# Kernel optimization log

Measured on AMD Instinct MI355X. Metric: run time of the kernel, lower is better.

The kernel has to match this reference:

```python
import jax, jax.numpy as jnp
import numpy as np

N = 200000      # total nodes
E = 3200000     # total edges (avg degree 16)
B = 2000        # graphs
NPG = 100       # nodes per graph (N = B*NPG)
H = 32          # hidden_channels
MAXZ = 1000     # max_z
K = 60          # sort-pool k
D = H * 3 + 1   # total_latent_dim = 97
DENSE = ((K - 2) // 2 + 1 - 5 + 1) * 32  # 832


def setup_inputs() -> dict:
    key = jax.random.key(0)
    ks = jax.random.split(key, 24)
    inp = {}
    inp['z1'] = jax.random.randint(ks[0], (N,), 0, MAXZ)
    inp['z2'] = jax.random.randint(ks[1], (N,), 0, MAXZ)
    inp['w'] = jax.random.randint(ks[2], (N,), 0, MAXZ)
    inp['edge_index'] = jax.random.randint(ks[3], (2, E), 0, N)
    inp['batch'] = jnp.arange(N) // NPG  # contiguous graph ids
    inp['edge_weight'] = jax.random.uniform(ks[4], (E,), dtype=jnp.float32)
    s = 0.1
    inp['emb_w'] = jax.random.normal(ks[5], (MAXZ, H), jnp.float32) * s
    inp['emb_z1'] = jax.random.normal(ks[6], (MAXZ, H), jnp.float32) * s
    inp['emb_z2'] = jax.random.normal(ks[7], (MAXZ, H), jnp.float32) * s
    inp['W0'] = jax.random.normal(ks[8], (3 * H, H), jnp.float32) * s
    inp['b0'] = jnp.zeros((H,), jnp.float32)
    inp['W1'] = jax.random.normal(ks[9], (H, H), jnp.float32) * s
    inp['b1'] = jnp.zeros((H,), jnp.float32)
    inp['W2'] = jax.random.normal(ks[10], (H, H), jnp.float32) * s
    inp['b2'] = jnp.zeros((H,), jnp.float32)
    inp['W3'] = jax.random.normal(ks[11], (H, 1), jnp.float32) * s
    inp['b3'] = jnp.zeros((1,), jnp.float32)
    inp['c1_W'] = jax.random.normal(ks[12], (16, 1, D), jnp.float32) * s
    inp['c1_b'] = jnp.zeros((16,), jnp.float32)
    inp['c2_W'] = jax.random.normal(ks[13], (32, 16, 5), jnp.float32) * s
    inp['c2_b'] = jnp.zeros((32,), jnp.float32)
    inp['l1_W'] = jax.random.normal(ks[14], (DENSE, 128), jnp.float32) * s
    inp['l1_b'] = jnp.zeros((128,), jnp.float32)
    inp['l2_W'] = jax.random.normal(ks[15], (128, 1), jnp.float32) * s
    inp['l2_b'] = jnp.zeros((1,), jnp.float32)
    return inp


def _gcn(x, W, b, src, dst, ew):
    # GCNConv: add self loops (weight 1), symmetric normalization, aggregate src->dst
    loop = jnp.arange(N)
    s = jnp.concatenate([src, loop])
    d = jnp.concatenate([dst, loop])
    wgt = jnp.concatenate([ew, jnp.ones((N,), ew.dtype)])
    deg = jax.ops.segment_sum(wgt, d, num_segments=N)
    dis = jnp.where(deg > 0, jax.lax.rsqrt(deg), 0.0)
    norm = dis[s] * wgt * dis[d]
    h = x @ W                                  # [N, out]
    out = jax.ops.segment_sum(norm[:, None] * h[s], d, num_segments=N)
    return out + b


def reference(z1, z2, w, edge_index, batch, edge_weight,
              emb_w, emb_z1, emb_z2,
              W0, b0, W1, b1, W2, b2, W3, b3,
              c1_W, c1_b, c2_W, c2_b, l1_W, l1_b, l2_W, l2_b):
    src, dst = edge_index[0], edge_index[1]
    x0 = jnp.concatenate([emb_w[w], emb_z1[z1], emb_z2[z2]], axis=1)  # [N, 3H]
    h1 = jnp.tanh(_gcn(x0, W0, b0, src, dst, edge_weight))
    h2 = jnp.tanh(_gcn(h1, W1, b1, src, dst, edge_weight))
    h3 = jnp.tanh(_gcn(h2, W2, b2, src, dst, edge_weight))
    h4 = jnp.tanh(_gcn(h3, W3, b3, src, dst, edge_weight))
    x = jnp.concatenate([h1, h2, h3, h4], axis=-1)  # [N, D]

    # global_sort_pool: contiguous equal-size graphs -> reshape, sort desc by last channel, top-k
    xg = x.reshape(B, NPG, D)
    order = jnp.argsort(-xg[..., -1], axis=1)[:, :K]          # [B, K]
    xk = jnp.take_along_axis(xg, order[..., None], axis=1)    # [B, K, D]

    # conv1: kernel=stride=D on flattened [B,1,K*D] == per-slot projection
    t = jax.nn.relu(jnp.einsum('bkd,od->bok', xk, c1_W[:, 0, :]) + c1_b[None, :, None])  # [B,16,K]
    t = t.reshape(B, 16, K // 2, 2).max(axis=-1)              # maxpool 2,2 -> [B,16,30]
    t = jax.lax.conv_general_dilated(t, c2_W, (1,), 'VALID',
                                     dimension_numbers=('NCH', 'OIH', 'NCH'))
    t = jax.nn.relu(t + c2_b[None, :, None])                  # [B,32,26]
    t = t.reshape(B, -1)                                      # [B, DENSE]
    t = jax.nn.relu(t @ l1_W + l1_b)
    # dropout p=0.5 skipped (eval mode)
    return t @ l2_W + l2_b                                    # [B,1]
```

## Files before the change

### kernel.cpp

```cpp
#include <hip/hip_runtime.h>
#include <math.h>

#define NPG 100
#define KTOP 60
#define DLAT 97
#define NC 250
#define NODESC 800
#define NBLKA 1024

static __device__ __forceinline__ float dot4(float4 a, float4 b){
  return a.x*b.x + a.y*b.y + a.z*b.z + a.w*b.w;
}

__global__ __launch_bounds__(256) void k_histA(const int* __restrict__ dst, int* __restrict__ histA,
    int E, int cpb){
  __shared__ int h[NC];
  int blk = blockIdx.x, tid = threadIdx.x;
  if(tid < NC) h[tid] = 0;
  __syncthreads();
  int e0 = blk*cpb, e1 = min(e0+cpb, E);
  for(int e=e0+tid; e<e1; e+=256) atomicAdd(&h[dst[e]/NODESC], 1);
  __syncthreads();
  if(tid < NC) histA[blk*NC + tid] = h[tid];
}

__global__ __launch_bounds__(NBLKA) void k_colscanA(const int* __restrict__ histA,
    int* __restrict__ prefA, int* __restrict__ totalA){
  __shared__ int s[NBLKA];
  int c = blockIdx.x, t = threadIdx.x;
  int v = histA[t*NC + c];
  s[t] = v;
  __syncthreads();
  for(int off=1; off<NBLKA; off<<=1){
    int u = (t >= off) ? s[t-off] : 0;
    __syncthreads();
    s[t] += u;
    __syncthreads();
  }
  prefA[c*NBLKA + t] = s[t] - v;
  if(t == NBLKA-1) totalA[c] = s[t];
}

__global__ __launch_bounds__(256) void k_bscanA(const int* __restrict__ totalA, int* __restrict__ cbase){
  __shared__ int s[256];
  int t = threadIdx.x;
  int v = (t < NC) ? totalA[t] : 0;
  s[t] = v;
  __syncthreads();
  for(int off=1; off<256; off<<=1){
    int u = (t >= off) ? s[t-off] : 0;
    __syncthreads();
    s[t] += u;
    __syncthreads();
  }
  if(t < NC) cbase[t] = s[t] - v;
  if(t == 255) cbase[NC] = s[255];
}

__global__ __launch_bounds__(256) void k_scatterA(const int* __restrict__ src, const int* __restrict__ dst,
    const float* __restrict__ ew, const int* __restrict__ prefA, const int* __restrict__ cbase,
    int2* __restrict__ ebufA, int E, int cpb){
  __shared__ int cur[NC];
  int blk = blockIdx.x, tid = threadIdx.x;
  if(tid < NC) cur[tid] = prefA[tid*NBLKA + blk] + cbase[tid];
  __syncthreads();
  int e0 = blk*cpb, e1 = min(e0+cpb, E);
  for(int e=e0+tid; e<e1; e+=256){
    int d = dst[e];
    int c = d/NODESC;
    int dm = d - c*NODESC;
    int pos = atomicAdd(&cur[c], 1);
    ebufA[pos] = make_int2(src[e] | (dm<<18), __float_as_int(ew[e]));
  }
}

__global__ __launch_bounds__(1024) void k_bucket8(const int2* __restrict__ ebufA, const int* __restrict__ cbase,
    float* __restrict__ dis, int* __restrict__ rs, int2* __restrict__ csr, int N){
  __shared__ float degw[NODESC];
  __shared__ int cnt[NODESC];
  __shared__ int cur[NODESC];
  __shared__ int sc[1024];
  int c = blockIdx.x, tid = threadIdx.x;
  int n0 = c*NODESC;
  if(tid < NODESC){ degw[tid] = 0.f; cnt[tid] = 0; }
  __syncthreads();
  int e0 = cbase[c], e1 = cbase[c+1];
  for(int e=e0+tid; e<e1; e+=1024){
    int2 t = ebufA[e];
    int ld = ((unsigned)t.x)>>18;
    atomicAdd(&cnt[ld], 1);
    atomicAdd(&degw[ld], __int_as_float(t.y));
  }
  __syncthreads();
  if(tid < NODESC) dis[n0+tid] = rsqrtf(degw[tid] + 1.0f);
  sc[tid] = (tid < NODESC) ? cnt[tid] : 0;
  __syncthreads();
  for(int off=1; off<1024; off<<=1){
    int u = (tid >= off) ? sc[tid-off] : 0;
    __syncthreads();
    sc[tid] += u;
    __syncthreads();
  }
  if(tid < NODESC){
    int st = e0 + sc[tid] - cnt[tid];
    cur[tid] = st;
    rs[n0+tid] = st;
  }
  if(c == NC-1 && tid == 0) rs[N] = e1;
  __syncthreads();
  for(int e=e0+tid; e<e1; e+=1024){
    int2 t = ebufA[e];
    int ld = ((unsigned)t.x)>>18;
    int pos = atomicAdd(&cur[ld], 1);
    csr[pos] = make_int2(t.x & 0x3FFFF, t.y);
  }
}

__global__ __launch_bounds__(256) void k_gemm1(const int* __restrict__ wI, const int* __restrict__ z1I,
   const int* __restrict__ z2I,
   const float* __restrict__ embw, const float* __restrict__ embz1, const float* __restrict__ embz2,
   const float* __restrict__ W0, const float* __restrict__ dis, float* __restrict__ gx, int N){
  __shared__ __align__(16) float X[128][97];
  __shared__ __align__(16) float Ws[96*32];
  __shared__ int iw[128], i1[128], i2[128];
  int tid = threadIdx.x;
  int g0 = blockIdx.x*128;
  for(int i=tid;i<768;i+=256) ((float4*)Ws)[i] = ((const float4*)W0)[i];
  if(tid < 128){
    int gn = g0 + tid;
    bool ok = gn < N;
    iw[tid] = ok ? wI[gn]  : 0;
    i1[tid] = ok ? z1I[gn] : 0;
    i2[tid] = ok ? z2I[gn] : 0;
  }
  __syncthreads();
  for(int r=0;r<48;r++){
    int flat = r*256 + tid;
    int n = flat/96, c = flat - n*96;
    int gn = g0 + n;
    float val = 0.f;
    if(gn < N){
      if(c < 32)      val = embw [iw[n]*32 + c];
      else if(c < 64) val = embz1[i1[n]*32 + (c-32)];
      else            val = embz2[i2[n]*32 + (c-64)];
    }
    X[n][c] = val;
  }
  __syncthreads();
  int ng = tid>>3, chg = tid&7;
  float4 acc[4];
  #pragma unroll
  for(int j=0;j<4;j++) acc[j] = make_float4(0.f,0.f,0.f,0.f);
  #pragma unroll 4
  for(int i=0;i<96;i++){
    float4 wv = *(const float4*)&Ws[i*32 + chg*4];
    #pragma unroll
    for(int j=0;j<4;j++){
      float xv = X[ng*4+j][i];
      acc[j].x += xv*wv.x; acc[j].y += xv*wv.y; acc[j].z += xv*wv.z; acc[j].w += xv*wv.w;
    }
  }
  #pragma unroll
  for(int j=0;j<4;j++){
    int gn = g0 + ng*4 + j;
    if(gn < N){
      float dv = dis[gn];
      acc[j].x *= dv; acc[j].y *= dv; acc[j].z *= dv; acc[j].w *= dv;
      *(float4*)&gx[(size_t)gn*32 + chg*4] = acc[j];
    }
  }
}

__global__ __launch_bounds__(256) void k_gemm32(const float* __restrict__ xin, const float* __restrict__ W,
    const float* __restrict__ dis, float* __restrict__ gx, int N){
  __shared__ __align__(16) float X[128][33];
  __shared__ __align__(16) float Ws[32*32];
  int tid = threadIdx.x;
  int g0 = blockIdx.x*128;
  ((float4*)Ws)[tid] = ((const float4*)W)[tid];
  for(int r=0;r<4;r++){
    int f = r*256 + tid;
    int n = f>>3, c4 = f&7;
    int gn = g0 + n;
    float4 v = (gn < N) ? ((const float4*)(xin + (size_t)gn*32))[c4] : make_float4(0,0,0,0);
    float* xr = &X[n][c4*4];
    xr[0]=v.x; xr[1]=v.y; xr[2]=v.z; xr[3]=v.w;
  }
  __syncthreads();
  int ng = tid>>3, chg = tid&7;
  float4 acc[4];
  #pragma unroll
  for(int j=0;j<4;j++) acc[j] = make_float4(0.f,0.f,0.f,0.f);
  #pragma unroll 4
  for(int i=0;i<32;i++){
    float4 wv = *(const float4*)&Ws[i*32 + chg*4];
    #pragma unroll
    for(int j=0;j<4;j++){
      float xv = X[ng*4+j][i];
      acc[j].x += xv*wv.x; acc[j].y += xv*wv.y; acc[j].z += xv*wv.z; acc[j].w += xv*wv.w;
    }
  }
  #pragma unroll
  for(int j=0;j<4;j++){
    int gn = g0 + ng*4 + j;
    if(gn < N){
      float dv = dis[gn];
      acc[j].x *= dv; acc[j].y *= dv; acc[j].z *= dv; acc[j].w *= dv;
      *(float4*)&gx[(size_t)gn*32 + chg*4] = acc[j];
    }
  }
}

__global__ __launch_bounds__(256) void k_agg32(const float* __restrict__ g,
   const float* __restrict__ dis, const int* __restrict__ rs, const int2* __restrict__ csr,
   const float* __restrict__ bias, float* __restrict__ hout, int N){
  int wave = threadIdx.x >> 6;
  int lane = threadIdx.x & 63;
  int es = lane >> 3;
  int cg = lane & 7;
  int n = blockIdx.x*4 + wave;
  if(n >= N) return;
  int e0 = rs[n], e1 = rs[n+1];
  int deg = e1 - e0;
  int iters = (deg + 7) >> 3;
  float4 acc = make_float4(0.f,0.f,0.f,0.f);
  int e = e0 + es;
  int2 p = (e < e1) ? csr[e] : make_int2(0,0);
  for(int it=0; it<iters; ++it){
    int s = p.x;
    float w = __int_as_float(p.y);
    e += 8;
    int2 pn = (e < e1) ? csr[e] : make_int2(0,0);
    float4 v = ((const float4*)(g + (size_t)s*32))[cg];
    acc.x += w*v.x; acc.y += w*v.y; acc.z += w*v.z; acc.w += w*v.w;
    p = pn;
  }
  #pragma unroll
  for(int off=8; off<64; off<<=1){
    acc.x += __shfl_xor(acc.x, off);
    acc.y += __shfl_xor(acc.y, off);
    acc.z += __shfl_xor(acc.z, off);
    acc.w += __shfl_xor(acc.w, off);
  }
  float4 self = ((const float4*)(g + (size_t)n*32))[cg];
  float dn = dis[n];
  float4 bv = ((const float4*)bias)[cg];
  if(es == 0){
    float4 o;
    o.x = tanhf(dn*(acc.x + self.x) + bv.x);
    o.y = tanhf(dn*(acc.y + self.y) + bv.y);
    o.z = tanhf(dn*(acc.z + self.z) + bv.z);
    o.w = tanhf(dn*(acc.w + self.w) + bv.w);
    ((float4*)(hout + (size_t)n*32))[cg] = o;
  }
}

__global__ __launch_bounds__(256) void k_agg32v(const float* __restrict__ g,
   const float* __restrict__ dis, const int* __restrict__ rs, const int2* __restrict__ csr,
   const float* __restrict__ bias, const float* __restrict__ W3,
   float* __restrict__ hout, float* __restrict__ gv, int N){
  int wave = threadIdx.x >> 6;
  int lane = threadIdx.x & 63;
  int es = lane >> 3;
  int cg = lane & 7;
  int n = blockIdx.x*4 + wave;
  if(n >= N) return;
  int e0 = rs[n], e1 = rs[n+1];
  int deg = e1 - e0;
  int iters = (deg + 7) >> 3;
  float4 acc = make_float4(0.f,0.f,0.f,0.f);
  int e = e0 + es;
  int2 p = (e < e1) ? csr[e] : make_int2(0,0);
  for(int it=0; it<iters; ++it){
    int s = p.x;
    float w = __int_as_float(p.y);
    e += 8;
    int2 pn = (e < e1) ? csr[e] : make_int2(0,0);
    float4 v = ((const float4*)(g + (size_t)s*32))[cg];
    acc.x += w*v.x; acc.y += w*v.y; acc.z += w*v.z; acc.w += w*v.w;
    p = pn;
  }
  #pragma unroll
  for(int off=8; off<64; off<<=1){
    acc.x += __shfl_xor(acc.x, off);
    acc.y += __shfl_xor(acc.y, off);
    acc.z += __shfl_xor(acc.z, off);
    acc.w += __shfl_xor(acc.w, off);
  }
  float4 self = ((const float4*)(g + (size_t)n*32))[cg];
  float dn = dis[n];
  float4 bv = ((const float4*)bias)[cg];
  if(es == 0){
    float4 o;
    o.x = tanhf(dn*(acc.x + self.x) + bv.x);
    o.y = tanhf(dn*(acc.y + self.y) + bv.y);
    o.z = tanhf(dn*(acc.z + self.z) + bv.z);
    o.w = tanhf(dn*(acc.w + self.w) + bv.w);
    ((float4*)(hout + (size_t)n*32))[cg] = o;
    float4 w3v = *(const float4*)&W3[cg*4];
    float s = dot4(o, w3v);
    s += __shfl_xor(s, 1);
    s += __shfl_xor(s, 2);
    s += __shfl_xor(s, 4);
    if(cg == 0) gv[n] = s*dn;
  }
}

__global__ __launch_bounds__(256) void k_sortpool(const float* __restrict__ gv,
  const float* __restrict__ dis, const int* __restrict__ rs, const int2* __restrict__ csr,
  const float* __restrict__ b3,
  const float* __restrict__ h1,const float* __restrict__ h2,const float* __restrict__ h3,
  const float* __restrict__ c1W,const float* __restrict__ c1b,
  float* __restrict__ t2G, int N){
  __shared__ float v[128];
  __shared__ int ord[KTOP];
  __shared__ __align__(16) float xk[KTOP][100];
  __shared__ __align__(16) float c1Ws[16*100];
  __shared__ __align__(16) float t2s[480];
  int b = blockIdx.x, tid = threadIdx.x;
  int g0 = b*NPG;
  for(int i=tid;i<16*97;i+=256){ int o=i/97, d=i-o*97; c1Ws[o*100+d]=c1W[i]; }
  if(tid < 100){
    int n = g0 + tid;
    float acc = gv[n];
    int e0 = rs[n], e1 = rs[n+1];
    for(int e=e0;e<e1;e++){
      int2 p = csr[e];
      acc += __int_as_float(p.y)*gv[p.x];
    }
    v[tid] = tanhf(dis[n]*acc + b3[0]);
  }
  __syncthreads();
  if(tid < 100){
    float vi = v[tid];
    int rank = 0;
    for(int j=0;j<100;j++){
      float vj = v[j];
      rank += (vj > vi) || (vj == vi && j < tid);
    }
    if(rank < KTOP) ord[rank] = tid;
  }
  __syncthreads();
  for(int idx=tid; idx<KTOP*DLAT; idx+=256){
    int k = idx/DLAT, d = idx - k*DLAT;
    int nk = ord[k];
    float val;
    if(d < 96){
      const float* hsrc = (d<32) ? h1 : (d<64) ? h2 : h3;
      val = hsrc[(size_t)(g0+nk)*32 + (d&31)];
    } else val = v[nk];
    xk[k][d] = val;
  }
  __syncthreads();
  {
    int og = tid & 7, j = tid >> 3;
    if(j < 30){
      int k0 = 2*j, k1 = 2*j+1;
      float a00=0.f, a01=0.f, a10=0.f, a11=0.f;
      for(int d=0; d<96; d+=4){
        float4 w0 = *(const float4*)&c1Ws[og*100 + d];
        float4 w1 = *(const float4*)&c1Ws[(og+8)*100 + d];
        float4 x0 = *(const float4*)&xk[k0][d];
        float4 x1 = *(const float4*)&xk[k1][d];
        a00 += dot4(x0, w0); a01 += dot4(x1, w0);
        a10 += dot4(x0, w1); a11 += dot4(x1, w1);
      }
      {
        float w0 = c1Ws[og*100 + 96], w1 = c1Ws[(og+8)*100 + 96];
        float x0 = xk[k0][96], x1 = xk[k1][96];
        a00 += x0*w0; a01 += x1*w0;
        a10 += x0*w1; a11 += x1*w1;
      }
      float b0v = c1b[og], b1v = c1b[og+8];
      float r0 = fmaxf(fmaxf(a00+b0v,0.f), fmaxf(a01+b0v,0.f));
      float r1 = fmaxf(fmaxf(a10+b1v,0.f), fmaxf(a11+b1v,0.f));
      t2s[og*30 + j] = r0;
      t2s[(og+8)*30 + j] = r1;
    }
  }
  __syncthreads();
  if(tid < 120) ((float4*)&t2G[(size_t)b*480])[tid] = ((const float4*)t2s)[tid];
}

__global__ __launch_bounds__(256) void k_tail(const float* __restrict__ t2G,
  const float* __restrict__ c2W,const float* __restrict__ c2b,
  const float* __restrict__ l1W,const float* __restrict__ l1b,
  const float* __restrict__ l2W,const float* __restrict__ l2b,
  float* __restrict__ out){
  __shared__ __align__(16) float t2s[8*480];
  __shared__ __align__(16) float c2Ws[2560];
  __shared__ __align__(16) float flat[8][832];
  __shared__ __align__(16) float o1s[8][128];
  int bG = blockIdx.x, tid = threadIdx.x;
  for(int i=tid; i<960; i+=256) ((float4*)t2s)[i] = ((const float4*)(t2G + (size_t)bG*8*480))[i];
  for(int i=tid; i<640; i+=256) ((float4*)c2Ws)[i] = ((const float4*)c2W)[i];
  __syncthreads();
  {
    int g = tid >> 5, oc = tid & 31;
    float acc[26];
    #pragma unroll
    for(int p=0;p<26;p++) acc[p]=0.f;
    for(int ic=0; ic<16; ic++){
      const float* trow = &t2s[g*480 + ic*30];
      float t[30];
      #pragma unroll
      for(int p=0;p<30;p++) t[p] = trow[p];
      const float* wr = &c2Ws[(oc*16 + ic)*5];
      float w0=wr[0], w1=wr[1], w2=wr[2], w3=wr[3], w4=wr[4];
      #pragma unroll
      for(int p=0;p<26;p++)
        acc[p] += t[p]*w0 + t[p+1]*w1 + t[p+2]*w2 + t[p+3]*w3 + t[p+4]*w4;
    }
    float bb = c2b[oc];
    #pragma unroll
    for(int p=0;p<26;p++) flat[g][oc*26+p] = fmaxf(acc[p]+bb, 0.f);
  }
  __syncthreads();
  {
    int j = tid & 127, gq = tid >> 7;
    float acc0=0.f, acc1=0.f, acc2=0.f, acc3=0.f;
    const float* f0 = flat[gq*4+0];
    const float* f1 = flat[gq*4+1];
    const float* f2 = flat[gq*4+2];
    const float* f3 = flat[gq*4+3];
    for(int i4=0; i4<208; i4++){
      int i = i4*4;
      float w0 = l1W[(size_t)i*128 + j];
      float w1 = l1W[(size_t)(i+1)*128 + j];
      float w2 = l1W[(size_t)(i+2)*128 + j];
      float w3 = l1W[(size_t)(i+3)*128 + j];
      float4 a0 = *(const float4*)&f0[i];
      float4 a1 = *(const float4*)&f1[i];
      float4 a2 = *(const float4*)&f2[i];
      float4 a3 = *(const float4*)&f3[i];
      acc0 += a0.x*w0 + a0.y*w1 + a0.z*w2 + a0.w*w3;
      acc1 += a1.x*w0 + a1.y*w1 + a1.z*w2 + a1.w*w3;
      acc2 += a2.x*w0 + a2.y*w1 + a2.z*w2 + a2.w*w3;
      acc3 += a3.x*w0 + a3.y*w1 + a3.z*w2 + a3.w*w3;
    }
    o1s[gq*4+0][j] = acc0;
    o1s[gq*4+1][j] = acc1;
    o1s[gq*4+2][j] = acc2;
    o1s[gq*4+3][j] = acc3;
  }
  __syncthreads();
  {
    int g = tid >> 5, jj = tid & 31;
    float s = 0.f;
    #pragma unroll
    for(int q=0;q<4;q++){
      int j = jj + 32*q;
      float r = fmaxf(o1s[g][j] + l1b[j], 0.f);
      s += r * l2W[j];
    }
    #pragma unroll
    for(int off=16; off>0; off>>=1) s += __shfl_xor(s, off);
    if(jj == 0) out[bG*8 + g] = s + l2b[0];
  }
}

extern "C" void kernel_launch(void* const* d_in, const int* in_sizes, int n_in,
                              void* d_out, int out_size, void* d_ws, size_t ws_size,
                              hipStream_t stream){
  (void)n_in; (void)out_size; (void)ws_size;
  const int*   z1    = (const int*)  d_in[0];
  const int*   z2    = (const int*)  d_in[1];
  const int*   w     = (const int*)  d_in[2];
  const int*   eidx  = (const int*)  d_in[3];
  const float* ew    = (const float*)d_in[5];
  const float* embw  = (const float*)d_in[6];
  const float* embz1 = (const float*)d_in[7];
  const float* embz2 = (const float*)d_in[8];
  const float* W0    = (const float*)d_in[9];
  const float* b0    = (const float*)d_in[10];
  const float* W1    = (const float*)d_in[11];
  const float* b1    = (const float*)d_in[12];
  const float* W2    = (const float*)d_in[13];
  const float* b2    = (const float*)d_in[14];
  const float* W3    = (const float*)d_in[15];
  const float* b3    = (const float*)d_in[16];
  const float* c1W   = (const float*)d_in[17];
  const float* c1b   = (const float*)d_in[18];
  const float* c2W   = (const float*)d_in[19];
  const float* c2b   = (const float*)d_in[20];
  const float* l1W   = (const float*)d_in[21];
  const float* l1b   = (const float*)d_in[22];
  const float* l2W   = (const float*)d_in[23];
  const float* l2b   = (const float*)d_in[24];
  float* out = (float*)d_out;

  int N = in_sizes[0];
  int E = in_sizes[3]/2;
  int B = N/NPG;
  const int* src = eidx;
  const int* dst = eidx + E;

  char* p = (char*)d_ws;
  auto alloc = [&](size_t bytes)->char*{
    char* r = p;
    p += (bytes + 255) & ~(size_t)255;
    return r;
  };
  float* h1    = (float*)alloc((size_t)N*32*4);
  float* h2    = (float*)alloc((size_t)N*32*4);
  float* h3    = (float*)alloc((size_t)N*32*4);
  float* gv    = (float*)alloc((size_t)N*4);
  float* gx    = (float*)alloc((size_t)N*32*4);
  float* dis   = (float*)alloc((size_t)N*4);
  int*   rs    = (int*)  alloc((size_t)(N+1)*4);
  int*   histA = (int*)  alloc((size_t)NBLKA*NC*4);
  int*   prefA = (int*)  alloc((size_t)NC*NBLKA*4);
  int*   totalA= (int*)  alloc((size_t)NC*4);
  int*   cbase = (int*)  alloc((size_t)(NC+1)*4);
  int2*  csr   = (int2*) alloc((size_t)E*8);
  float* t2G   = (float*)alloc((size_t)B*480*4);
  int2*  ebufA = (int2*)h1;

  int cpb = (E + NBLKA - 1)/NBLKA;
  k_histA   <<<NBLKA, 256, 0, stream>>>(dst, histA, E, cpb);
  k_colscanA<<<NC, NBLKA, 0, stream>>>(histA, prefA, totalA);
  k_bscanA  <<<1,    256, 0, stream>>>(totalA, cbase);
  k_scatterA<<<NBLKA, 256, 0, stream>>>(src, dst, ew, prefA, cbase, ebufA, E, cpb);
  k_bucket8 <<<NC,  1024, 0, stream>>>(ebufA, cbase, dis, rs, csr, N);

  int gG = (N+127)/128;
  int gA = (N+3)/4;
  k_gemm1 <<<gG, 256, 0, stream>>>(w, z1, z2, embw, embz1, embz2, W0, dis, gx, N);
  k_agg32 <<<gA, 256, 0, stream>>>(gx, dis, rs, csr, b0, h1, N);
  k_gemm32<<<gG, 256, 0, stream>>>(h1, W1, dis, gx, N);
  k_agg32 <<<gA, 256, 0, stream>>>(gx, dis, rs, csr, b1, h2, N);
  k_gemm32<<<gG, 256, 0, stream>>>(h2, W2, dis, gx, N);
  k_agg32v<<<gA, 256, 0, stream>>>(gx, dis, rs, csr, b2, W3, h3, gv, N);

  k_sortpool<<<B, 256, 0, stream>>>(gv, dis, rs, csr, b3, h1, h2, h3, c1W, c1b, t2G, N);
  k_tail    <<<B/8, 256, 0, stream>>>(t2G, c2W, c2b, l1W, l1b, l2W, l2b, out);
}
```

Baseline: 691.9 us.

## Pre-scale CSR source to byte offsets, transpose histogram, shrink partition block count

```diff
diff --git a/kernel.cpp b/kernel.cpp
--- a/kernel.cpp
+++ b/kernel.cpp
@@ -6,13 +6,13 @@
 #define DLAT 97
 #define NC 250
 #define NODESC 800
-#define NBLKA 1024
+#define NBLKA 256
 
 static __device__ __forceinline__ float dot4(float4 a, float4 b){
   return a.x*b.x + a.y*b.y + a.z*b.z + a.w*b.w;
 }
 
-__global__ __launch_bounds__(256) void k_histA(const int* __restrict__ dst, int* __restrict__ histA,
+__global__ __launch_bounds__(256) void k_histA(const int* __restrict__ dst, int* __restrict__ histT,
     int E, int cpb){
   __shared__ int h[NC];
   int blk = blockIdx.x, tid = threadIdx.x;
@@ -21,14 +21,14 @@
   int e0 = blk*cpb, e1 = min(e0+cpb, E);
   for(int e=e0+tid; e<e1; e+=256) atomicAdd(&h[dst[e]/NODESC], 1);
   __syncthreads();
-  if(tid < NC) histA[blk*NC + tid] = h[tid];
-}
-
-__global__ __launch_bounds__(NBLKA) void k_colscanA(const int* __restrict__ histA,
+  if(tid < NC) histT[tid*NBLKA + blk] = h[tid];
+}
+
+__global__ __launch_bounds__(NBLKA) void k_colscanA(const int* __restrict__ histT,
     int* __restrict__ prefA, int* __restrict__ totalA){
   __shared__ int s[NBLKA];
   int c = blockIdx.x, t = threadIdx.x;
-  int v = histA[t*NC + c];
+  int v = histT[c*NBLKA + t];
   s[t] = v;
   __syncthreads();
   for(int off=1; off<NBLKA; off<<=1){
@@ -112,7 +112,7 @@
     int2 t = ebufA[e];
     int ld = ((unsigned)t.x)>>18;
     int pos = atomicAdd(&cur[ld], 1);
-    csr[pos] = make_int2(t.x & 0x3FFFF, t.y);
+    csr[pos] = make_int2((t.x & 0x3FFFF) << 7, t.y);
   }
 }
 
@@ -222,18 +222,23 @@
   if(n >= N) return;
   int e0 = rs[n], e1 = rs[n+1];
   int deg = e1 - e0;
-  int iters = (deg + 7) >> 3;
+  int full = deg >> 3, rem = deg & 7;
+  const char* gb = (const char*)g;
+  int cgo = cg*16;
   float4 acc = make_float4(0.f,0.f,0.f,0.f);
-  int e = e0 + es;
-  int2 p = (e < e1) ? csr[e] : make_int2(0,0);
-  for(int it=0; it<iters; ++it){
-    int s = p.x;
+  int idx = e0 + es;
+  for(int it=0; it<full; ++it){
+    int2 p = csr[idx];
     float w = __int_as_float(p.y);
-    e += 8;
-    int2 pn = (e < e1) ? csr[e] : make_int2(0,0);
-    float4 v = ((const float4*)(g + (size_t)s*32))[cg];
+    float4 v = *(const float4*)(gb + (p.x + cgo));
     acc.x += w*v.x; acc.y += w*v.y; acc.z += w*v.z; acc.w += w*v.w;
-    p = pn;
+    idx += 8;
+  }
+  if(es < rem){
+    int2 p = csr[idx];
+    float w = __int_as_float(p.y);
+    float4 v = *(const float4*)(gb + (p.x + cgo));
+    acc.x += w*v.x; acc.y += w*v.y; acc.z += w*v.z; acc.w += w*v.w;
   }
   #pragma unroll
   for(int off=8; off<64; off<<=1){
@@ -267,18 +272,23 @@
   if(n >= N) return;
   int e0 = rs[n], e1 = rs[n+1];
   int deg = e1 - e0;
-  int iters = (deg + 7) >> 3;
+  int full = deg >> 3, rem = deg & 7;
+  const char* gb = (const char*)g;
+  int cgo = cg*16;
   float4 acc = make_float4(0.f,0.f,0.f,0.f);
-  int e = e0 + es;
-  int2 p = (e < e1) ? csr[e] : make_int2(0,0);
-  for(int it=0; it<iters; ++it){
-    int s = p.x;
+  int idx = e0 + es;
+  for(int it=0; it<full; ++it){
+    int2 p = csr[idx];
     float w = __int_as_float(p.y);
-    e += 8;
-    int2 pn = (e < e1) ? csr[e] : make_int2(0,0);
-    float4 v = ((const float4*)(g + (size_t)s*32))[cg];
+    float4 v = *(const float4*)(gb + (p.x + cgo));
     acc.x += w*v.x; acc.y += w*v.y; acc.z += w*v.z; acc.w += w*v.w;
-    p = pn;
+    idx += 8;
+  }
+  if(es < rem){
+    int2 p = csr[idx];
+    float w = __int_as_float(p.y);
+    float4 v = *(const float4*)(gb + (p.x + cgo));
+    acc.x += w*v.x; acc.y += w*v.y; acc.z += w*v.z; acc.w += w*v.w;
   }
   #pragma unroll
   for(int off=8; off<64; off<<=1){
@@ -326,7 +336,7 @@
     int e0 = rs[n], e1 = rs[n+1];
     for(int e=e0;e<e1;e++){
       int2 p = csr[e];
-      acc += __int_as_float(p.y)*gv[p.x];
+      acc += __int_as_float(p.y)*gv[((unsigned)p.x)>>7];
     }
     v[tid] = tanhf(dis[n]*acc + b3[0]);
   }
@@ -508,7 +518,7 @@
   float* gx    = (float*)alloc((size_t)N*32*4);
   float* dis   = (float*)alloc((size_t)N*4);
   int*   rs    = (int*)  alloc((size_t)(N+1)*4);
-  int*   histA = (int*)  alloc((size_t)NBLKA*NC*4);
+  int*   histT = (int*)  alloc((size_t)NBLKA*NC*4);
   int*   prefA = (int*)  alloc((size_t)NC*NBLKA*4);
   int*   totalA= (int*)  alloc((size_t)NC*4);
   int*   cbase = (int*)  alloc((size_t)(NC+1)*4);
@@ -517,8 +527,8 @@
   int2*  ebufA = (int2*)h1;
 
   int cpb = (E + NBLKA - 1)/NBLKA;
-  k_histA   <<<NBLKA, 256, 0, stream>>>(dst, histA, E, cpb);
-  k_colscanA<<<NC, NBLKA, 0, stream>>>(histA, prefA, totalA);
+  k_histA   <<<NBLKA, 256, 0, stream>>>(dst, histT, E, cpb);
+  k_colscanA<<<NC, NBLKA, 0, stream>>>(histT, prefA, totalA);
   k_bscanA  <<<1,    256, 0, stream>>>(totalA, cbase);
   k_scatterA<<<NBLKA, 256, 0, stream>>>(src, dst, ew, prefA, cbase, ebufA, E, cpb);
   k_bucket8 <<<NC,  1024, 0, stream>>>(ebufA, cbase, dis, rs, csr, N);
```

Measured after the change: 706.0 us. 1.02x slower.
